# Optimization experiments

Measured on AMD Instinct MI355X. Metric: run time of the kernel, lower is better.

The kernel has to match this reference:

```python
import jax, jax.numpy as jnp
import numpy as np

N_NODES = 100000


def _gcn_norm(edge_index, num_nodes):
    # Add self-loops, then symmetric normalization D^-1/2 A D^-1/2 (PyG gcn_norm).
    loops = jnp.arange(num_nodes, dtype=edge_index.dtype)
    src = jnp.concatenate([edge_index[0], loops])
    dst = jnp.concatenate([edge_index[1], loops])
    ew = jnp.ones(src.shape[0], dtype=jnp.float32)
    deg = jax.ops.segment_sum(ew, dst, num_segments=num_nodes)
    dinv = jnp.where(deg > 0, jax.lax.rsqrt(deg), 0.0)
    norm = dinv[src] * ew * dinv[dst]
    return src, dst, norm


def _prop_gcn_conv(x, W, b, src, dst, norm, num_nodes, prop_nums):
    # PropGCNConv: linear transform once, then prop_nums hops of normalized
    # sparse propagation (gather from src, scale, scatter-add to dst), + bias.
    x = x @ W
    for _ in range(prop_nums):
        msgs = x[src] * norm[:, None]              # [E, d]
        x = jax.ops.segment_sum(msgs, dst, num_segments=num_nodes)
    return x + b


def setup_inputs() -> dict:
    key = jax.random.key(0)
    k1, k2, k3, k4 = jax.random.split(key, 4)
    in_dim, hid_dim, num_classes = 128, 64, 40
    n_edges = 800000
    x = jax.random.normal(k1, (N_NODES, in_dim), dtype=jnp.float32)
    W0 = jax.random.normal(k2, (in_dim, hid_dim), dtype=jnp.float32) * (1.0 / np.sqrt(in_dim))
    b0 = jnp.zeros((hid_dim,), dtype=jnp.float32)
    Wc = jax.random.normal(k3, (hid_dim, num_classes), dtype=jnp.float32) * (1.0 / np.sqrt(hid_dim))
    bc = jnp.zeros((num_classes,), dtype=jnp.float32)
    edge_index = jax.random.randint(k4, (2, n_edges), 0, N_NODES, dtype=jnp.int64)
    return {"x": x, "W0": W0, "b0": b0, "Wc": Wc, "bc": bc,
            "edge_index": edge_index, "prop_nums": 30}


def reference(x, W0, b0, Wc, bc, edge_index, prop_nums):
    n = x.shape[0]
    src, dst, norm = _gcn_norm(edge_index, n)
    # feat_bottleneck: conv -> relu -> dropout (eval mode -> identity)
    h = _prop_gcn_conv(x, W0, b0, src, dst, norm, n, prop_nums)
    h = jax.nn.relu(h)
    # feat_classifier: single-hop PropGCNConv
    out = _prop_gcn_conv(h, Wc, bc, src, dst, norm, n, 1)
    return out
```

## Files before the change

### kernel.cpp

```cpp
#include <hip/hip_runtime.h>

#define NN  100000
#define NE  800000
#define NNZ 900000
#define IN_DIM 128
#define HID 64
#define NC  40
#define HOPS 30

typedef _Float16 half8 __attribute__((ext_vector_type(8)));


__global__ void count_edges_k(const int* __restrict__ dst, int* __restrict__ cnt) {
    int e = blockIdx.x * blockDim.x + threadIdx.x;
    if (e < NE) atomicAdd(&cnt[dst[e]], 1);
}

__global__ void dinv_k(const int* __restrict__ cnt, float* __restrict__ dinv) {
    int i = blockIdx.x * blockDim.x + threadIdx.x;
    if (i < NN) dinv[i] = rsqrtf((float)(cnt[i] + 1));
}

__global__ void scan_blocks_k(const int* __restrict__ cnt, int* __restrict__ rp,
                              int* __restrict__ partials) {
    __shared__ int s[256];
    int tid = threadIdx.x;
    int i = blockIdx.x * 256 + tid;
    int v = (i < NN) ? (cnt[i] + 1) : 0;
    s[tid] = v;
    __syncthreads();
    for (int off = 1; off < 256; off <<= 1) {
        int t = (tid >= off) ? s[tid - off] : 0;
        __syncthreads();
        s[tid] += t;
        __syncthreads();
    }
    if (i < NN) rp[i] = s[tid] - v;
    if (tid == 255) partials[blockIdx.x] = s[255];
}

__global__ void scan_partials_k(int* __restrict__ partials, int nblk) {
    __shared__ int s[512];
    int tid = threadIdx.x;
    int v = (tid < nblk) ? partials[tid] : 0;
    s[tid] = v;
    __syncthreads();
    for (int off = 1; off < 512; off <<= 1) {
        int t = (tid >= off) ? s[tid - off] : 0;
        __syncthreads();
        s[tid] += t;
        __syncthreads();
    }
    if (tid < nblk) partials[tid] = s[tid] - v;
}

__global__ void add_offsets_k(int* __restrict__ rp, const int* __restrict__ partials) {
    int i = blockIdx.x * 256 + threadIdx.x;
    if (i < NN) rp[i] += partials[blockIdx.x];
    if (i == 0) rp[NN] = NNZ;
}

__global__ void fill_csr_k(const int* __restrict__ src, const int* __restrict__ dst,
                           const float* __restrict__ dinv, const int* __restrict__ rp,
                           int* __restrict__ cnt, int2* __restrict__ cv) {
    int e = blockIdx.x * blockDim.x + threadIdx.x;
    if (e >= NNZ) return;
    int pos;
    int2 p;
    if (e < NE) {
        int s = src[e], d = dst[e];
        int old = atomicAdd(&cnt[d], -1);
        pos = rp[d] + old - 1;
        p.x = s;
        p.y = __float_as_int(dinv[s] * dinv[d]);
    } else {
        int i = e - NE;
        pos = rp[i + 1] - 1;
        p.x = i;
        p.y = __float_as_int(dinv[i] * dinv[i]);
    }
    cv[pos] = p;
}


__global__ void __launch_bounds__(256) gemm1_k(const float* __restrict__ x,
                                               const float* __restrict__ W,
                                               _Float16* __restrict__ out) {
    int t = threadIdx.x;
    int cq = __builtin_amdgcn_readfirstlane(t >> 6);
    int node = blockIdx.x * 64 + (t & 63);
    int nc = node < NN ? node : NN - 1;
    const float4* xr = (const float4*)(x + (size_t)nc * IN_DIM);
    const float* Wq = W + cq * 16;
    float acc[16];
#pragma unroll
    for (int c = 0; c < 16; ++c) acc[c] = 0.f;
#pragma unroll 4
    for (int k4 = 0; k4 < IN_DIM / 4; ++k4) {
        float4 xv = xr[k4];
#pragma unroll
        for (int kk = 0; kk < 4; ++kk) {
            float xs = (kk == 0) ? xv.x : (kk == 1) ? xv.y : (kk == 2) ? xv.z : xv.w;
            const float4* wr = (const float4*)(Wq + (k4 * 4 + kk) * HID);
#pragma unroll
            for (int c4 = 0; c4 < 4; ++c4) {
                float4 wv = wr[c4];
                acc[c4 * 4 + 0] = fmaf(xs, wv.x, acc[c4 * 4 + 0]);
                acc[c4 * 4 + 1] = fmaf(xs, wv.y, acc[c4 * 4 + 1]);
                acc[c4 * 4 + 2] = fmaf(xs, wv.z, acc[c4 * 4 + 2]);
                acc[c4 * 4 + 3] = fmaf(xs, wv.w, acc[c4 * 4 + 3]);
            }
        }
    }
    if (node < NN) {
        half8* o = (half8*)(out + (size_t)node * HID + cq * 16);
        half8 r0, r1;
#pragma unroll
        for (int j = 0; j < 8; ++j) {
            r0[j] = (_Float16)acc[j];
            r1[j] = (_Float16)acc[j + 8];
        }
        o[0] = r0;
        o[1] = r1;
    }
}

__global__ void prop64_k(const _Float16* __restrict__ xin, _Float16* __restrict__ xout,
                         const int* __restrict__ rp, const int2* __restrict__ cv) {
    int wid  = threadIdx.x >> 6;
    int lane = threadIdx.x & 63;
    int n    = lane >> 5;
    int s    = (lane >> 3) & 3;
    int f    = lane & 7;
    int node = blockIdx.x * 8 + wid * 2 + n;
    int beg = rp[node], end = rp[node + 1];
    const half8* x8 = (const half8*)xin;
    float a0 = 0.f, a1 = 0.f, a2 = 0.f, a3 = 0.f, a4 = 0.f, a5 = 0.f, a6 = 0.f, a7 = 0.f;
    for (int e = beg + s; e < end; e += 16) {
        int  e1 = e + 4,  e2 = e + 8,  e3 = e + 12;
        bool p1 = e1 < end, p2 = e2 < end, p3 = e3 < end;
        int2 q0 = cv[e];
        int2 q1 = cv[p1 ? e1 : beg];
        int2 q2 = cv[p2 ? e2 : beg];
        int2 q3 = cv[p3 ? e3 : beg];
        float v0 = __int_as_float(q0.y);
        float v1 = p1 ? __int_as_float(q1.y) : 0.f;
        float v2 = p2 ? __int_as_float(q2.y) : 0.f;
        float v3 = p3 ? __int_as_float(q3.y) : 0.f;
        half8 x0 = x8[(size_t)q0.x * 8 + f];
        half8 x1 = x8[(size_t)q1.x * 8 + f];
        half8 x2 = x8[(size_t)q2.x * 8 + f];
        half8 x3 = x8[(size_t)q3.x * 8 + f];
        a0 += v0 * (float)x0[0] + v1 * (float)x1[0] + v2 * (float)x2[0] + v3 * (float)x3[0];
        a1 += v0 * (float)x0[1] + v1 * (float)x1[1] + v2 * (float)x2[1] + v3 * (float)x3[1];
        a2 += v0 * (float)x0[2] + v1 * (float)x1[2] + v2 * (float)x2[2] + v3 * (float)x3[2];
        a3 += v0 * (float)x0[3] + v1 * (float)x1[3] + v2 * (float)x2[3] + v3 * (float)x3[3];
        a4 += v0 * (float)x0[4] + v1 * (float)x1[4] + v2 * (float)x2[4] + v3 * (float)x3[4];
        a5 += v0 * (float)x0[5] + v1 * (float)x1[5] + v2 * (float)x2[5] + v3 * (float)x3[5];
        a6 += v0 * (float)x0[6] + v1 * (float)x1[6] + v2 * (float)x2[6] + v3 * (float)x3[6];
        a7 += v0 * (float)x0[7] + v1 * (float)x1[7] + v2 * (float)x2[7] + v3 * (float)x3[7];
    }
#pragma unroll
    for (int m = 8; m <= 16; m <<= 1) {
        a0 += __shfl_xor(a0, m); a1 += __shfl_xor(a1, m);
        a2 += __shfl_xor(a2, m); a3 += __shfl_xor(a3, m);
        a4 += __shfl_xor(a4, m); a5 += __shfl_xor(a5, m);
        a6 += __shfl_xor(a6, m); a7 += __shfl_xor(a7, m);
    }
    if (s == 0) {
        half8 r;
        r[0] = (_Float16)a0; r[1] = (_Float16)a1; r[2] = (_Float16)a2; r[3] = (_Float16)a3;
        r[4] = (_Float16)a4; r[5] = (_Float16)a5; r[6] = (_Float16)a6; r[7] = (_Float16)a7;
        ((half8*)xout)[(size_t)node * 8 + f] = r;
    }
}

__global__ void __launch_bounds__(256, 4) gemm2_k(const _Float16* __restrict__ h,
                                                  const float* __restrict__ b0,
                                                  const float* __restrict__ Wc,
                                                  _Float16* __restrict__ g) {
    __shared__ float Wcs[HID * NC];
    __shared__ float b0s[HID];
    int t = threadIdx.x;
    for (int i = t; i < HID * NC / 4; i += 256)
        ((float4*)Wcs)[i] = ((const float4*)Wc)[i];
    if (t < HID) b0s[t] = b0[t];
    __syncthreads();
    int node = blockIdx.x * 256 + t;
    if (node >= NN) return;
    const half8* hr = (const half8*)(h + (size_t)node * HID);
    float acc[NC];
#pragma unroll
    for (int c = 0; c < NC; ++c) acc[c] = 0.f;
#pragma unroll
    for (int j = 0; j < 8; ++j) {
        half8 hv = hr[j];
#pragma unroll
        for (int m = 0; m < 8; ++m) {
            int k = j * 8 + m;
            float fv = fmaxf((float)hv[m] + b0s[k], 0.f);
            const float4* wr = (const float4*)(Wcs + k * NC);
#pragma unroll
            for (int c4 = 0; c4 < NC / 4; ++c4) {
                float4 wv = wr[c4];
                acc[c4 * 4 + 0] = fmaf(fv, wv.x, acc[c4 * 4 + 0]);
                acc[c4 * 4 + 1] = fmaf(fv, wv.y, acc[c4 * 4 + 1]);
                acc[c4 * 4 + 2] = fmaf(fv, wv.z, acc[c4 * 4 + 2]);
                acc[c4 * 4 + 3] = fmaf(fv, wv.w, acc[c4 * 4 + 3]);
            }
        }
    }
    half8* go = (half8*)(g + (size_t)node * NC);
#pragma unroll
    for (int j = 0; j < 5; ++j) {
        half8 r;
#pragma unroll
        for (int m = 0; m < 8; ++m) r[m] = (_Float16)acc[j * 8 + m];
        go[j] = r;
    }
}

__global__ void prop40_k(const _Float16* __restrict__ g, float* __restrict__ out,
                         const int* __restrict__ rp, const int2* __restrict__ cv,
                         const float* __restrict__ bc) {
    int t = blockIdx.x * 256 + threadIdx.x;
    int node = t >> 6;
    int lane = threadIdx.x & 63;
    int s = lane >> 3;
    int f = lane & 7;
    int beg = rp[node], end = rp[node + 1];
    const half8* g8 = (const half8*)g;
    bool act = f < 5;
    float a0 = 0.f, a1 = 0.f, a2 = 0.f, a3 = 0.f, a4 = 0.f, a5 = 0.f, a6 = 0.f, a7 = 0.f;
    for (int e = beg + s; e < end; e += 16) {
        int  e1 = e + 8;
        bool p1 = e1 < end;
        int2 q0 = cv[e];
        int2 q1 = cv[p1 ? e1 : beg];
        float v0 = __int_as_float(q0.y);
        float v1 = p1 ? __int_as_float(q1.y) : 0.f;
        if (act) {
            half8 x0 = g8[(size_t)q0.x * 5 + f];
            half8 x1 = g8[(size_t)q1.x * 5 + f];
            a0 += v0 * (float)x0[0] + v1 * (float)x1[0];
            a1 += v0 * (float)x0[1] + v1 * (float)x1[1];
            a2 += v0 * (float)x0[2] + v1 * (float)x1[2];
            a3 += v0 * (float)x0[3] + v1 * (float)x1[3];
            a4 += v0 * (float)x0[4] + v1 * (float)x1[4];
            a5 += v0 * (float)x0[5] + v1 * (float)x1[5];
            a6 += v0 * (float)x0[6] + v1 * (float)x1[6];
            a7 += v0 * (float)x0[7] + v1 * (float)x1[7];
        }
    }
#pragma unroll
    for (int m = 8; m <= 32; m <<= 1) {
        a0 += __shfl_xor(a0, m); a1 += __shfl_xor(a1, m);
        a2 += __shfl_xor(a2, m); a3 += __shfl_xor(a3, m);
        a4 += __shfl_xor(a4, m); a5 += __shfl_xor(a5, m);
        a6 += __shfl_xor(a6, m); a7 += __shfl_xor(a7, m);
    }
    if (s == 0 && act) {
        float* o = out + (size_t)node * NC + f * 8;
        o[0] = a0 + bc[f * 8 + 0];
        o[1] = a1 + bc[f * 8 + 1];
        o[2] = a2 + bc[f * 8 + 2];
        o[3] = a3 + bc[f * 8 + 3];
        o[4] = a4 + bc[f * 8 + 4];
        o[5] = a5 + bc[f * 8 + 5];
        o[6] = a6 + bc[f * 8 + 6];
        o[7] = a7 + bc[f * 8 + 7];
    }
}


extern "C" void kernel_launch(void* const* d_in, const int* in_sizes, int n_in,
                              void* d_out, int out_size, void* d_ws, size_t ws_size,
                              hipStream_t stream) {
    const float* x  = (const float*)d_in[0];
    const float* W0 = (const float*)d_in[1];
    const float* b0 = (const float*)d_in[2];
    const float* Wc = (const float*)d_in[3];
    const float* bc = (const float*)d_in[4];
    const int*   ei = (const int*)d_in[5];
    const int* src = ei;
    const int* dst = ei + NE;

    char* ws = (char*)d_ws;
    size_t off = 0;
    auto alloc = [&](size_t bytes) -> void* {
        void* p = ws + off;
        off = (off + bytes + 255) & ~(size_t)255;
        return p;
    };
    float* dinv     = (float*)alloc((size_t)NN * 4);
    int*   rp       = (int*)  alloc((size_t)(NN + 1) * 4);
    int*   cnt      = (int*)  alloc((size_t)NN * 4);
    int*   partials = (int*)  alloc(512 * 4);
    int2*  cvp      = (int2*) alloc((size_t)NNZ * 8);
    _Float16* XA    = (_Float16*)alloc((size_t)NN * HID * 2);
    _Float16* XB    = (_Float16*)alloc((size_t)NN * HID * 2);
    _Float16* G     = (_Float16*)alloc((size_t)NN * NC * 2);

    const int nblk_n = (NN + 255) / 256;

    hipMemsetAsync(cnt, 0, (size_t)NN * 4, stream);
    count_edges_k<<<(NE + 255) / 256, 256, 0, stream>>>(dst, cnt);
    dinv_k       <<<nblk_n, 256, 0, stream>>>(cnt, dinv);
    scan_blocks_k<<<nblk_n, 256, 0, stream>>>(cnt, rp, partials);
    scan_partials_k<<<1, 512, 0, stream>>>(partials, nblk_n);
    add_offsets_k<<<nblk_n, 256, 0, stream>>>(rp, partials);
    fill_csr_k   <<<(NNZ + 255) / 256, 256, 0, stream>>>(src, dst, dinv, rp, cnt, cvp);

    gemm1_k<<<(NN + 63) / 64, 256, 0, stream>>>(x, W0, XA);

    _Float16* a = XA;
    _Float16* b = XB;
    for (int hop = 0; hop < HOPS; ++hop) {
        prop64_k<<<NN / 8, 256, 0, stream>>>(a, b, rp, cvp);
        _Float16* tmp = a; a = b; b = tmp;
    }

    gemm2_k<<<nblk_n, 256, 0, stream>>>(a, b0, Wc, G);
    prop40_k<<<NN * HID / 256, 256, 0, stream>>>(G, (float*)d_out, rp, cvp, bc);
}
```

Before: 836.0 us.

## Build CSR in two passes via 256-node bucket scatter then finalize

Replaces the single-pass CSR fill, which scattered entries to random positions with per-node atomics, with two passes. The first pass scatters (src,dst) pairs into 256-node buckets using per-bucket atomic cursors. The second pass reads the buckets in order, places each entry within its row and computes the normalization weight. This aims to localize atomics and writes during CSR construction. The cost is an extra kernel launch, a temporary buffer and an extra pass over roughly 7MB.

```diff
diff --git a/kernel.cpp b/kernel.cpp
--- a/kernel.cpp
+++ b/kernel.cpp
@@ -60,25 +60,30 @@
     if (i == 0) rp[NN] = NNZ;
 }
 
-__global__ void fill_csr_k(const int* __restrict__ src, const int* __restrict__ dst,
-                           const float* __restrict__ dinv, const int* __restrict__ rp,
-                           int* __restrict__ cnt, int2* __restrict__ cv) {
+__global__ void scatter_k(const int* __restrict__ src, const int* __restrict__ dst,
+                          const int* __restrict__ rp, int* __restrict__ bcur,
+                          int2* __restrict__ tmp) {
     int e = blockIdx.x * blockDim.x + threadIdx.x;
     if (e >= NNZ) return;
-    int pos;
-    int2 p;
-    if (e < NE) {
-        int s = src[e], d = dst[e];
-        int old = atomicAdd(&cnt[d], -1);
-        pos = rp[d] + old - 1;
-        p.x = s;
-        p.y = __float_as_int(dinv[s] * dinv[d]);
-    } else {
-        int i = e - NE;
-        pos = rp[i + 1] - 1;
-        p.x = i;
-        p.y = __float_as_int(dinv[i] * dinv[i]);
-    }
+    int s, d;
+    if (e < NE) { s = src[e]; d = dst[e]; }
+    else        { s = d = e - NE; }
+    int b = d >> 8;
+    int pos = rp[d & ~255] + atomicAdd(&bcur[b], 1);
+    int2 t; t.x = s; t.y = d;
+    tmp[pos] = t;
+}
+
+__global__ void finalize_k(const int2* __restrict__ tmp, const int* __restrict__ rp,
+                           int* __restrict__ cnt, const float* __restrict__ dinv,
+                           int2* __restrict__ cv) {
+    int e = blockIdx.x * blockDim.x + threadIdx.x;
+    if (e >= NNZ) return;
+    int2 t = tmp[e];
+    int s = t.x, d = t.y;
+    int old = atomicAdd(&cnt[d], -1);
+    int pos = rp[d] + old;
+    int2 p; p.x = s; p.y = __float_as_int(dinv[s] * dinv[d]);
     cv[pos] = p;
 }
 
@@ -296,20 +301,25 @@
     int*   rp       = (int*)  alloc((size_t)(NN + 1) * 4);
     int*   cnt      = (int*)  alloc((size_t)NN * 4);
     int*   partials = (int*)  alloc(512 * 4);
+    int*   bcur     = (int*)  alloc(512 * 4);
+    int2*  tmp      = (int2*) alloc((size_t)NNZ * 8);
     int2*  cvp      = (int2*) alloc((size_t)NNZ * 8);
     _Float16* XA    = (_Float16*)alloc((size_t)NN * HID * 2);
     _Float16* XB    = (_Float16*)alloc((size_t)NN * HID * 2);
     _Float16* G     = (_Float16*)alloc((size_t)NN * NC * 2);
 
     const int nblk_n = (NN + 255) / 256;
+    const int nblk_z = (NNZ + 255) / 256;
 
     hipMemsetAsync(cnt, 0, (size_t)NN * 4, stream);
+    hipMemsetAsync(bcur, 0, 512 * 4, stream);
     count_edges_k<<<(NE + 255) / 256, 256, 0, stream>>>(dst, cnt);
     dinv_k       <<<nblk_n, 256, 0, stream>>>(cnt, dinv);
     scan_blocks_k<<<nblk_n, 256, 0, stream>>>(cnt, rp, partials);
     scan_partials_k<<<1, 512, 0, stream>>>(partials, nblk_n);
     add_offsets_k<<<nblk_n, 256, 0, stream>>>(rp, partials);
-    fill_csr_k   <<<(NNZ + 255) / 256, 256, 0, stream>>>(src, dst, dinv, rp, cnt, cvp);
+    scatter_k    <<<nblk_z, 256, 0, stream>>>(src, dst, rp, bcur, tmp);
+    finalize_k   <<<nblk_z, 256, 0, stream>>>(tmp, rp, cnt, dinv, cvp);
 
     gemm1_k<<<(NN + 63) / 64, 256, 0, stream>>>(x, W0, XA);
 
@@ -317,7 +327,7 @@
     _Float16* b = XB;
     for (int hop = 0; hop < HOPS; ++hop) {
         prop64_k<<<NN / 8, 256, 0, stream>>>(a, b, rp, cvp);
-        _Float16* tmp = a; a = b; b = tmp;
+        _Float16* tmp2 = a; a = b; b = tmp2;
     }
 
     gemm2_k<<<nblk_n, 256, 0, stream>>>(a, b0, Wc, G);
```

Result: slower. 1.196 ms (+43.0%).
